# Kernel optimization log

Measured on AMD Instinct MI355X. Metric: run time of the kernel, lower is better.

The kernel has to match this reference:

```python
import jax, jax.numpy as jnp
import numpy as np

B, Q, K, D, H, HD, OUT = 4, 1024, 1024, 256, 8, 32, 256


def setup_inputs() -> dict:
    key = jax.random.key(0)
    ks = jax.random.split(key, 11)
    s = 0.05  # small init scale for weights
    return {
        "q_data": jax.random.normal(ks[0], (B, Q, D), jnp.float32),
        "m_data": jax.random.normal(ks[1], (B, K, D), jnp.float32),
        "bias": jax.random.normal(ks[2], (B, 1, 1, K), jnp.float32),
        "nonbatched_bias": jax.random.normal(ks[3], (H, Q, K), jnp.float32),
        "query_w": jax.random.normal(ks[4], (D, H, HD), jnp.float32) * s,
        "key_w": jax.random.normal(ks[5], (D, H, HD), jnp.float32) * s,
        "value_w": jax.random.normal(ks[6], (D, H, HD), jnp.float32) * s,
        "gating_w": jax.random.normal(ks[7], (D, H, HD), jnp.float32) * s,
        "gating_b": jnp.ones((H, HD), jnp.float32),
        "output_w": jax.random.normal(ks[8], (H, HD, OUT), jnp.float32) * s,
        "output_b": jnp.zeros((OUT,), jnp.float32),
    }


def reference(q_data, m_data, bias, nonbatched_bias, query_w, key_w, value_w,
              gating_w, gating_b, output_w, output_b):
    key_dim = query_w.shape[-1]
    # QKV projections; queries pre-scaled by 1/sqrt(head_dim)
    q = jnp.einsum('bqa,ahc->bqhc', q_data, query_w) * key_dim ** (-0.5)
    k = jnp.einsum('bka,ahc->bkhc', m_data, key_w)
    v = jnp.einsum('bka,ahc->bkhc', m_data, value_w)
    # attention logits [b,h,q,k] plus batched and nonbatched additive biases
    logits_update = jnp.einsum('bqhc,bkhc->bhqk', q, k)
    logits = logits_update + bias + nonbatched_bias[None]
    weights = jax.nn.softmax(logits, axis=-1)
    weighted_avg = jnp.einsum('bhqk,bkhc->bqhc', weights, v)
    # sigmoid gating on the value-aggregated output
    gate = jax.nn.sigmoid(jnp.einsum('bqc,chv->bqhv', q_data, gating_w) + gating_b)
    weighted_avg = weighted_avg * gate
    output = jnp.einsum('bqhc,hco->bqo', weighted_avg, output_w) + output_b
    return (output, logits_update)
```

## Files before the change

### kernel.cpp

```cpp
#include <hip/hip_runtime.h>
#include <hip/hip_bf16.h>

#define NB 4
#define NQ 1024
#define NKS 1024
#define ND 256
#define NH 8
#define NHD 32
#define NOUT 256
#define SPLIT 4

typedef __attribute__((ext_vector_type(8))) short v8s;
typedef __attribute__((ext_vector_type(4))) short v4s;
typedef __attribute__((ext_vector_type(4))) float f32x4;

__global__ __launch_bounds__(256) void prep_all(
    const float* __restrict__ qd, const float* __restrict__ md,
    const float* __restrict__ qw, const float* __restrict__ kw,
    const float* __restrict__ vw, const float* __restrict__ gw,
    const float* __restrict__ ow,
    __hip_bfloat16* __restrict__ Abf, __hip_bfloat16* __restrict__ Wt)
{
  if (blockIdx.x < 1024) {
    const int gid = blockIdx.x * 256 + threadIdx.x;
    const float* src = (gid < 131072) ? qd : md;
    const size_t off = (size_t)(gid & 131071) * 8;
    const float4 a = ((const float4*)(src + off))[0];
    const float4 c = ((const float4*)(src + off))[1];
    __hip_bfloat16 t8[8];
    t8[0]=__float2bfloat16(a.x); t8[1]=__float2bfloat16(a.y);
    t8[2]=__float2bfloat16(a.z); t8[3]=__float2bfloat16(a.w);
    t8[4]=__float2bfloat16(c.x); t8[5]=__float2bfloat16(c.y);
    t8[6]=__float2bfloat16(c.z); t8[7]=__float2bfloat16(c.w);
    *(v8s*)(Abf + (size_t)gid * 8) = *(v8s*)t8;
    return;
  }
  __shared__ float tile[64][65];
  const int wb = blockIdx.x - 1024;
  const int m = wb >> 4, bx = wb & 15;
  const float* src = (m == 0) ? qw : (m == 1) ? kw : (m == 2) ? vw
                   : (m == 3) ? gw : ow;
  const float scale = (m == 0) ? 0.1767766952966369f : 1.0f;
  const int d0 = (bx >> 2) * 64, o0 = (bx & 3) * 64;
  #pragma unroll
  for (int i = 0; i < 16; ++i) {
    const int idx = threadIdx.x + i * 256;
    tile[idx >> 6][idx & 63] = src[(size_t)(d0 + (idx >> 6)) * 256 + o0 + (idx & 63)];
  }
  __syncthreads();
  __hip_bfloat16* dst = Wt + (size_t)m * 65536;
  #pragma unroll
  for (int i = 0; i < 16; ++i) {
    const int idx = threadIdx.x + i * 256;
    const int orow = idx >> 6, dc = idx & 63;
    dst[(size_t)(o0 + orow) * 256 + d0 + dc] = __float2bfloat16(tile[dc][orow] * scale);
  }
}

__global__ __launch_bounds__(256) void proj_kernel(
    const __hip_bfloat16* __restrict__ Abf, const __hip_bfloat16* __restrict__ Wt,
    const float* __restrict__ gating_b,
    __hip_bfloat16* __restrict__ Qw, __hip_bfloat16* __restrict__ Kw,
    __hip_bfloat16* __restrict__ Vt, __hip_bfloat16* __restrict__ G)
{
  const int wv = threadIdx.x >> 6, lane = threadIdx.x & 63;
  const int c = lane & 15, g = lane >> 4;
  const int task = blockIdx.x * 4 + wv;
  const int ctg = task & 3;
  const int mat = (task >> 2) & 1;
  const int r0g = (task >> 3) & 255;
  const int src = task >> 11;
  const int r0 = r0g * 16;
  const int b = r0 >> 10, pos0 = r0 & 1023;
  const f32x4 z = {0.f, 0.f, 0.f, 0.f};

  const __hip_bfloat16* A = Abf + ((size_t)src * 4096 + r0) * 256;
  v8s af[8];
  #pragma unroll
  for (int ks = 0; ks < 8; ++ks)
    af[ks] = *(const v8s*)(A + c * 256 + ks * 32 + g * 8);

  const int widx = (src == 0) ? (mat ? 3 : 0) : (mat ? 2 : 1);
  const __hip_bfloat16* W = Wt + (size_t)widx * 65536;
  const bool swapped = (src == 1) && (mat == 1);

  f32x4 ac[4] = {z, z, z, z};
  #pragma unroll
  for (int ks = 0; ks < 8; ++ks) {
    #pragma unroll
    for (int j = 0; j < 4; ++j) {
      v8s wf = *(const v8s*)(W + (size_t)((ctg * 4 + j) * 16 + c) * 256 + ks * 32 + g * 8);
      ac[j] = swapped
        ? __builtin_amdgcn_mfma_f32_16x16x32_bf16(wf, af[ks], ac[j], 0, 0, 0)
        : __builtin_amdgcn_mfma_f32_16x16x32_bf16(af[ks], wf, ac[j], 0, 0, 0);
    }
  }

  if (src == 0 && mat == 0) {
    #pragma unroll
    for (int j = 0; j < 4; ++j) {
      const int o = (ctg * 4 + j) * 16 + c, h = o >> 5, hd = o & 31;
      #pragma unroll
      for (int r = 0; r < 4; ++r)
        Qw[((size_t)(b * NH + h) * 1024 + pos0 + 4 * g + r) * 32 + hd] =
            __float2bfloat16(ac[j][r]);
    }
  } else if (src == 0) {
    #pragma unroll
    for (int j = 0; j < 4; ++j) {
      const int o = (ctg * 4 + j) * 16 + c;
      const float gb = gating_b[o];
      #pragma unroll
      for (int r = 0; r < 4; ++r)
        G[(size_t)(r0 + 4 * g + r) * 256 + o] = __float2bfloat16(ac[j][r] + gb);
    }
  } else if (mat == 0) {
    #pragma unroll
    for (int j = 0; j < 4; ++j) {
      const int o = (ctg * 4 + j) * 16 + c, h = o >> 5, hd = o & 31;
      #pragma unroll
      for (int r = 0; r < 4; ++r)
        Kw[((size_t)(b * NH + h) * 1024 + pos0 + 4 * g + r) * 32 + hd] =
            __float2bfloat16(ac[j][r]);
    }
  } else {
    #pragma unroll
    for (int j = 0; j < 4; ++j) {
      #pragma unroll
      for (int r = 0; r < 4; ++r) {
        const int o2 = (ctg * 4 + j) * 16 + 4 * g + r;
        Vt[((size_t)(b * NH + (o2 >> 5)) * 32 + (o2 & 31)) * 1024 + pos0 + c] =
            __float2bfloat16(ac[j][r]);
      }
    }
  }
}

__global__ __launch_bounds__(256) void attn_kernel(
    const __hip_bfloat16* __restrict__ Qw, const __hip_bfloat16* __restrict__ Kw,
    const __hip_bfloat16* __restrict__ Vt,
    const float* __restrict__ bias, const float* __restrict__ nbb,
    float* __restrict__ out_logits,
    __hip_bfloat16* __restrict__ partO, float* __restrict__ partL)
{
  __shared__ __align__(16) __hip_bfloat16 sP[4][16][72];

  const int wv = threadIdx.x >> 6, lane = threadIdx.x & 63;
  const int c = lane & 15, g = lane >> 4;
  const int xcd   = blockIdx.x & 7;
  const int slot  = blockIdx.x >> 3;
  const int bh    = ((slot >> 6) << 3) | xcd;
  const int inner = slot & 63;
  const int sp    = inner >> 4;
  const int qtg   = inner & 15;
  const int qt  = qtg * 4 + wv;
  const int b = bh >> 3, h = bh & 7;
  const int rem = bh * 64 + qt;
  const int q0 = qt * 16;
  const int kbase = sp * (NKS / SPLIT);
  const size_t bhs = (size_t)bh;

  const __hip_bfloat16* Kbase = Kw + bhs * NKS * NHD;
  const __hip_bfloat16* Vbase = Vt + bhs * NHD * NKS;
  const float* biasb = bias + (size_t)b * NKS;
  const float* nbbb  = nbb + ((size_t)h * NQ + q0) * NKS;

  const v8s qfrag = *(const v8s*)(Qw + (bhs * NQ + q0 + c) * NHD + g * 8);

  const f32x4 zacc = {0.f, 0.f, 0.f, 0.f};
  f32x4 O0 = zacc, O1 = zacc;
  float lsumL[4] = {0.f, 0.f, 0.f, 0.f};

  auto loadKV = [&](int k0, v8s* kf, v8s* vf) {
    kf[0] = *(const v8s*)(Kbase + (k0 +      c) * NHD + g * 8);
    kf[1] = *(const v8s*)(Kbase + (k0 + 16 + c) * NHD + g * 8);
    kf[2] = *(const v8s*)(Kbase + (k0 + 32 + c) * NHD + g * 8);
    kf[3] = *(const v8s*)(Kbase + (k0 + 48 + c) * NHD + g * 8);
    vf[0] = *(const v8s*)(Vbase + (     c) * NKS + k0 +      g * 8);
    vf[1] = *(const v8s*)(Vbase + (16 + c) * NKS + k0 +      g * 8);
    vf[2] = *(const v8s*)(Vbase + (     c) * NKS + k0 + 32 + g * 8);
    vf[3] = *(const v8s*)(Vbase + (16 + c) * NKS + k0 + 32 + g * 8);
  };
  auto loadBias = [&](int k0, float* bn) {
    #pragma unroll
    for (int t = 0; t < 4; ++t) {
      const float bvt = biasb[k0 + t * 16 + c];
      #pragma unroll
      for (int r = 0; r < 4; ++r)
        bn[t * 4 + r] = bvt + nbbb[(g * 4 + r) * NKS + k0 + t * 16 + c];
    }
  };

  auto compute = [&](int k0, const v8s* kf, const v8s* vf, const float* bn) {
    f32x4 S[4];
    #pragma unroll
    for (int t = 0; t < 4; ++t)
      S[t] = __builtin_amdgcn_mfma_f32_16x16x32_bf16(qfrag, kf[t], zacc, 0, 0, 0);

    #pragma unroll
    for (int r = 0; r < 4; ++r) {
      const int qrow = q0 + g * 4 + r;
      float* lp = out_logits + (bhs * NQ + qrow) * (size_t)NKS + k0 + c;
      float psum = 0.f;
      #pragma unroll
      for (int t = 0; t < 4; ++t) {
        lp[t * 16] = S[t][r];
        const float p = __expf(S[t][r] + bn[t * 4 + r]);
        psum += p;
        sP[wv][g * 4 + r][t * 16 + c] = __float2bfloat16(p);
      }
      lsumL[r] += psum;
    }

    const v8s pa0 = *(const v8s*)&sP[wv][c][g * 8];
    const v8s pa1 = *(const v8s*)&sP[wv][c][32 + g * 8];
    O0 = __builtin_amdgcn_mfma_f32_16x16x32_bf16(pa0, vf[0], O0, 0, 0, 0);
    O0 = __builtin_amdgcn_mfma_f32_16x16x32_bf16(pa1, vf[2], O0, 0, 0, 0);
    O1 = __builtin_amdgcn_mfma_f32_16x16x32_bf16(pa0, vf[1], O1, 0, 0, 0);
    O1 = __builtin_amdgcn_mfma_f32_16x16x32_bf16(pa1, vf[3], O1, 0, 0, 0);
  };

  v8s kfA[4], vfA[4], kfB[4], vfB[4];
  float bnA[16], bnB[16];

  loadKV(kbase, kfA, vfA);
  loadBias(kbase, bnA);
  #pragma unroll 1
  for (int kt = 0; kt < NKS / SPLIT / 64; kt += 2) {
    loadKV(kbase + (kt + 1) * 64, kfB, vfB);
    loadBias(kbase + (kt + 1) * 64, bnB);
    compute(kbase + kt * 64, kfA, vfA, bnA);
    if (kt + 2 < NKS / SPLIT / 64) {
      loadKV(kbase + (kt + 2) * 64, kfA, vfA);
      loadBias(kbase + (kt + 2) * 64, bnA);
    }
    compute(kbase + (kt + 1) * 64, kfB, vfB, bnB);
  }

  #pragma unroll
  for (int r = 0; r < 4; ++r) {
    float rs = lsumL[r];
    rs += __shfl_xor(rs, 1);
    rs += __shfl_xor(rs, 2);
    rs += __shfl_xor(rs, 4);
    rs += __shfl_xor(rs, 8);
    const int row = 4 * g + r;
    const size_t pb = ((size_t)(rem * SPLIT + sp) * 16 + row) * 32;
    partO[pb + c]      = __float2bfloat16(O0[r]);
    partO[pb + 16 + c] = __float2bfloat16(O1[r]);
    if (c == 0) partL[(size_t)(rem * SPLIT + sp) * 16 + row] = rs;
  }
}

__global__ __launch_bounds__(256) void outproj_kernel(
    const __hip_bfloat16* __restrict__ partO, const float* __restrict__ partL,
    const __hip_bfloat16* __restrict__ G, const __hip_bfloat16* __restrict__ WtO,
    const float* __restrict__ output_b, float* __restrict__ out)
{
  __shared__ __align__(16) __hip_bfloat16 sRows[16][264];
  const int t = threadIdx.x;
  const int wv = t >> 6, lane = t & 63;
  const int c = lane & 15, g = lane >> 4;
  const int r0 = blockIdx.x * 16;
  const int b = r0 >> 10, qt = (r0 & 1023) >> 4;
  const int h = t >> 5, hd = t & 31;
  const int rem = (b * NH + h) * 64 + qt;

  #pragma unroll 4
  for (int row = 0; row < 16; ++row) {
    float o = 0.f, l = 0.f;
    #pragma unroll
    for (int sp = 0; sp < SPLIT; ++sp) {
      const size_t base = (size_t)(rem * SPLIT + sp) * 16 + row;
      o += __bfloat162float(partO[base * 32 + hd]);
      l += partL[base];
    }
    const float gl = __bfloat162float(G[(size_t)(r0 + row) * 256 + t]);
    sRows[row][t] = __float2bfloat16((o / l) * (1.f / (1.f + __expf(-gl))));
  }
  __syncthreads();

  const f32x4 z = {0.f, 0.f, 0.f, 0.f};
  f32x4 ac[4] = {z, z, z, z};
  #pragma unroll
  for (int ks = 0; ks < 8; ++ks) {
    const v8s af = *(const v8s*)&sRows[c][ks * 32 + g * 8];
    #pragma unroll
    for (int j = 0; j < 4; ++j) {
      const v8s wf = *(const v8s*)(WtO + (size_t)((wv * 4 + j) * 16 + c) * 256 + ks * 32 + g * 8);
      ac[j] = __builtin_amdgcn_mfma_f32_16x16x32_bf16(af, wf, ac[j], 0, 0, 0);
    }
  }
  #pragma unroll
  for (int j = 0; j < 4; ++j) {
    const int o = (wv * 4 + j) * 16 + c;
    const float ob = output_b[o];
    #pragma unroll
    for (int r = 0; r < 4; ++r)
      out[(size_t)(r0 + 4 * g + r) * 256 + o] = ac[j][r] + ob;
  }
}

extern "C" void kernel_launch(void* const* d_in, const int* in_sizes, int n_in,
                              void* d_out, int out_size, void* d_ws, size_t ws_size,
                              hipStream_t stream) {
  const float* q_data   = (const float*)d_in[0];
  const float* m_data   = (const float*)d_in[1];
  const float* bias     = (const float*)d_in[2];
  const float* nbb      = (const float*)d_in[3];
  const float* query_w  = (const float*)d_in[4];
  const float* key_w    = (const float*)d_in[5];
  const float* value_w  = (const float*)d_in[6];
  const float* gating_w = (const float*)d_in[7];
  const float* gating_b = (const float*)d_in[8];
  const float* output_w = (const float*)d_in[9];
  const float* output_b = (const float*)d_in[10];

  float* out        = (float*)d_out;
  float* out_logits = out + (size_t)NB * NQ * NOUT;

  char* ws = (char*)d_ws;
  const size_t MB = 1u << 20;
  __hip_bfloat16* Qw  = (__hip_bfloat16*)(ws);
  __hip_bfloat16* Kw  = (__hip_bfloat16*)(ws + 2 * MB);
  __hip_bfloat16* Vt  = (__hip_bfloat16*)(ws + 4 * MB);
  __hip_bfloat16* G   = (__hip_bfloat16*)(ws + 6 * MB);
  __hip_bfloat16* Abf = (__hip_bfloat16*)(ws + 10 * MB);
  __hip_bfloat16* partO = (__hip_bfloat16*)(ws + 10 * MB);
  float*          partL = (float*)(ws + 19 * MB);
  __hip_bfloat16* Wt  = (__hip_bfloat16*)(ws + 20 * MB);

  prep_all<<<1104, 256, 0, stream>>>(q_data, m_data, query_w, key_w, value_w,
                                     gating_w, output_w, Abf, Wt);
  proj_kernel<<<1024, 256, 0, stream>>>(Abf, Wt, gating_b, Qw, Kw, Vt, G);
  attn_kernel<<<2048, 256, 0, stream>>>(Qw, Kw, Vt, bias, nbb, out_logits, partO, partL);
  outproj_kernel<<<256, 256, 0, stream>>>(partO, partL, G, Wt + (size_t)4 * 65536,
                                          output_b, out);
}
```

Baseline: 84.68 us.

## Remove key-split in attention and fuse gating normalization into its epilogue

Each attention block now processes the full key range instead of a quarter, so per-split partial outputs and row sums are no longer written and reduced. The softmax normalization and sigmoid gating move into the attention epilogue, which writes a gated bf16 weighted average directly. The output projection then reads that buffer with no reduction or shared-memory staging. The trade-off is a 4x smaller attention grid with longer serial loops per wave, which may reduce occupancy and latency hiding for the bandwidth-heavy bias and logits streams.

```diff
diff --git a/kernel.cpp b/kernel.cpp
--- a/kernel.cpp
+++ b/kernel.cpp
@@ -8,7 +8,6 @@
 #define NH 8
 #define NHD 32
 #define NOUT 256
-#define SPLIT 4
 
 typedef __attribute__((ext_vector_type(8))) short v8s;
 typedef __attribute__((ext_vector_type(4))) short v4s;
@@ -140,8 +139,8 @@
     const __hip_bfloat16* __restrict__ Qw, const __hip_bfloat16* __restrict__ Kw,
     const __hip_bfloat16* __restrict__ Vt,
     const float* __restrict__ bias, const float* __restrict__ nbb,
-    float* __restrict__ out_logits,
-    __hip_bfloat16* __restrict__ partO, float* __restrict__ partL)
+    const __hip_bfloat16* __restrict__ G,
+    float* __restrict__ out_logits, __hip_bfloat16* __restrict__ WA)
 {
   __shared__ __align__(16) __hip_bfloat16 sP[4][16][72];
 
@@ -149,15 +148,11 @@
   const int c = lane & 15, g = lane >> 4;
   const int xcd   = blockIdx.x & 7;
   const int slot  = blockIdx.x >> 3;
-  const int bh    = ((slot >> 6) << 3) | xcd;
-  const int inner = slot & 63;
-  const int sp    = inner >> 4;
-  const int qtg   = inner & 15;
+  const int bh    = ((slot >> 4) << 3) | xcd;
+  const int qtg   = slot & 15;
   const int qt  = qtg * 4 + wv;
   const int b = bh >> 3, h = bh & 7;
-  const int rem = bh * 64 + qt;
   const int q0 = qt * 16;
-  const int kbase = sp * (NKS / SPLIT);
   const size_t bhs = (size_t)bh;
 
   const __hip_bfloat16* Kbase = Kw + bhs * NKS * NHD;
@@ -223,18 +218,18 @@
   v8s kfA[4], vfA[4], kfB[4], vfB[4];
   float bnA[16], bnB[16];
 
-  loadKV(kbase, kfA, vfA);
-  loadBias(kbase, bnA);
+  loadKV(0, kfA, vfA);
+  loadBias(0, bnA);
   #pragma unroll 1
-  for (int kt = 0; kt < NKS / SPLIT / 64; kt += 2) {
-    loadKV(kbase + (kt + 1) * 64, kfB, vfB);
-    loadBias(kbase + (kt + 1) * 64, bnB);
-    compute(kbase + kt * 64, kfA, vfA, bnA);
-    if (kt + 2 < NKS / SPLIT / 64) {
-      loadKV(kbase + (kt + 2) * 64, kfA, vfA);
-      loadBias(kbase + (kt + 2) * 64, bnA);
-    }
-    compute(kbase + (kt + 1) * 64, kfB, vfB, bnB);
+  for (int kt = 0; kt < NKS / 64; kt += 2) {
+    loadKV((kt + 1) * 64, kfB, vfB);
+    loadBias((kt + 1) * 64, bnB);
+    compute(kt * 64, kfA, vfA, bnA);
+    if (kt + 2 < NKS / 64) {
+      loadKV((kt + 2) * 64, kfA, vfA);
+      loadBias((kt + 2) * 64, bnA);
+    }
+    compute((kt + 1) * 64, kfB, vfB, bnB);
   }
 
   #pragma unroll
@@ -244,47 +239,30 @@
     rs += __shfl_xor(rs, 2);
     rs += __shfl_xor(rs, 4);
     rs += __shfl_xor(rs, 8);
-    const int row = 4 * g + r;
-    const size_t pb = ((size_t)(rem * SPLIT + sp) * 16 + row) * 32;
-    partO[pb + c]      = __float2bfloat16(O0[r]);
-    partO[pb + 16 + c] = __float2bfloat16(O1[r]);
-    if (c == 0) partL[(size_t)(rem * SPLIT + sp) * 16 + row] = rs;
+    const float inv = 1.0f / rs;
+    const int qrow = q0 + g * 4 + r;
+    const size_t gb = ((size_t)b * NQ + qrow) * 256 + h * NHD;
+    const float gl0 = __bfloat162float(G[gb + c]);
+    const float gl1 = __bfloat162float(G[gb + 16 + c]);
+    WA[gb + c]      = __float2bfloat16(O0[r] * inv * (1.f / (1.f + __expf(-gl0))));
+    WA[gb + 16 + c] = __float2bfloat16(O1[r] * inv * (1.f / (1.f + __expf(-gl1))));
   }
 }
 
 __global__ __launch_bounds__(256) void outproj_kernel(
-    const __hip_bfloat16* __restrict__ partO, const float* __restrict__ partL,
-    const __hip_bfloat16* __restrict__ G, const __hip_bfloat16* __restrict__ WtO,
+    const __hip_bfloat16* __restrict__ WA, const __hip_bfloat16* __restrict__ WtO,
     const float* __restrict__ output_b, float* __restrict__ out)
 {
-  __shared__ __align__(16) __hip_bfloat16 sRows[16][264];
   const int t = threadIdx.x;
   const int wv = t >> 6, lane = t & 63;
   const int c = lane & 15, g = lane >> 4;
   const int r0 = blockIdx.x * 16;
-  const int b = r0 >> 10, qt = (r0 & 1023) >> 4;
-  const int h = t >> 5, hd = t & 31;
-  const int rem = (b * NH + h) * 64 + qt;
-
-  #pragma unroll 4
-  for (int row = 0; row < 16; ++row) {
-    float o = 0.f, l = 0.f;
-    #pragma unroll
-    for (int sp = 0; sp < SPLIT; ++sp) {
-      const size_t base = (size_t)(rem * SPLIT + sp) * 16 + row;
-      o += __bfloat162float(partO[base * 32 + hd]);
-      l += partL[base];
-    }
-    const float gl = __bfloat162float(G[(size_t)(r0 + row) * 256 + t]);
-    sRows[row][t] = __float2bfloat16((o / l) * (1.f / (1.f + __expf(-gl))));
-  }
-  __syncthreads();
 
   const f32x4 z = {0.f, 0.f, 0.f, 0.f};
   f32x4 ac[4] = {z, z, z, z};
   #pragma unroll
   for (int ks = 0; ks < 8; ++ks) {
-    const v8s af = *(const v8s*)&sRows[c][ks * 32 + g * 8];
+    const v8s af = *(const v8s*)(WA + (size_t)(r0 + c) * 256 + ks * 32 + g * 8);
     #pragma unroll
     for (int j = 0; j < 4; ++j) {
       const v8s wf = *(const v8s*)(WtO + (size_t)((wv * 4 + j) * 16 + c) * 256 + ks * 32 + g * 8);
@@ -326,14 +304,12 @@
   __hip_bfloat16* Vt  = (__hip_bfloat16*)(ws + 4 * MB);
   __hip_bfloat16* G   = (__hip_bfloat16*)(ws + 6 * MB);
   __hip_bfloat16* Abf = (__hip_bfloat16*)(ws + 10 * MB);
-  __hip_bfloat16* partO = (__hip_bfloat16*)(ws + 10 * MB);
-  float*          partL = (float*)(ws + 19 * MB);
+  __hip_bfloat16* WA  = (__hip_bfloat16*)(ws + 10 * MB);
   __hip_bfloat16* Wt  = (__hip_bfloat16*)(ws + 20 * MB);
 
   prep_all<<<1104, 256, 0, stream>>>(q_data, m_data, query_w, key_w, value_w,
                                      gating_w, output_w, Abf, Wt);
   proj_kernel<<<1024, 256, 0, stream>>>(Abf, Wt, gating_b, Qw, Kw, Vt, G);
-  attn_kernel<<<2048, 256, 0, stream>>>(Qw, Kw, Vt, bias, nbb, out_logits, partO, partL);
-  outproj_kernel<<<256, 256, 0, stream>>>(partO, partL, G, Wt + (size_t)4 * 65536,
-                                          output_b, out);
-}
+  attn_kernel<<<512, 256, 0, stream>>>(Qw, Kw, Vt, bias, nbb, G, out_logits, WA);
+  outproj_kernel<<<256, 256, 0, stream>>>(WA, Wt + (size_t)4 * 65536, output_b, out);
+}
```

Result: faster. 77.82 us (-8.1%).
